# Optimization experiments

Hardware: AMD Instinct MI355X
Metric: run time of the kernel (lower is better)

Reference implementation:

```python
import jax, jax.numpy as jnp
import numpy as np

B, D, SL, N, H, LL = 2, 128, 1024, 64, 4, 4
LN_EPS = 1e-5
DIST_EPS = 1e-8


def _ln(x, g, b):
    m = x.mean(-1, keepdims=True)
    v = ((x - m) ** 2).mean(-1, keepdims=True)
    return (x - m) / jnp.sqrt(v + LN_EPS) * g + b


def _sla(x, qw, qb, kw, kb, vw, vb, ow, ob):
    # x: [B, R, C, D]; rank-1 scaled linear attention (head_qk_dim = 1)
    Bq, R, C, Dd = x.shape
    Hh = qw.shape[0]
    hd = Dd // Hh
    q = jnp.einsum('brcd,hd->brhc', x, qw) + qb[:, None]   # [B,R,H,C]
    k = jnp.einsum('brcd,hd->brhc', x, kw) + kb[:, None]
    q = jax.nn.elu(q) + 1.0
    k = jax.nn.elu(k) + 1.0
    q = q / q.mean(-1, keepdims=True)
    k = k / k.sum(-1, keepdims=True)
    v = (jnp.einsum('brcd,ed->brce', x, vw) + vb).reshape(Bq, R, C, Hh, hd)
    v = v.transpose(0, 1, 3, 2, 4)                         # [B,R,H,C,hd]
    ktv = jnp.einsum('brhc,brhce->brhe', k, v)             # [B,R,H,hd]
    V = jnp.einsum('brhc,brhe->brche', q, ktv)             # [B,R,C,H,hd]
    V = V.reshape(Bq, R, C, Dd)
    return jnp.einsum('brcd,ed->brce', V, ow) + ob


def _forward(x, rq_w, rq_b, rk_w, rk_b, rv_w, rv_b, ro_w, ro_b,
             cq_w, cq_b, ck_w, ck_b, cv_w, cv_b, co_w, co_b,
             ln_r_g, ln_r_b, ln_c_g, ln_c_b, ln_f_g, ln_f_b,
             f1_w, f1_b, f2_w, f2_b):
    y = x.transpose(0, 2, 3, 1)   # [B, L, N, D] channels-last

    def layer(y, p):
        (rqw, rqb, rkw, rkb, rvw, rvb, row_, rob,
         cqw, cqb, ckw, ckb, cvw, cvb, cow, cob,
         lrg, lrb, lcg, lcb, lfg, lfb, f1w, f1b, f2w, f2b) = p
        # row attention: rows = L, cols = N
        y = y + _sla(_ln(y, lrg, lrb), rqw, rqb, rkw, rkb, rvw, rvb, row_, rob)
        # col attention: rows = N, cols = L
        hc = _ln(y, lcg, lcb).swapaxes(1, 2)
        y = y + _sla(hc, cqw, cqb, ckw, ckb, cvw, cvb, cow, cob).swapaxes(1, 2)
        # FFN (1x1 convs == pointwise linears)
        hf = _ln(y, lfg, lfb)
        hf = jax.nn.gelu(jnp.einsum('blnd,ed->blne', hf, f1w) + f1b, approximate=False)
        y = y + (jnp.einsum('blne,de->blnd', hf, f2w) + f2b)
        return y, None

    params = (rq_w, rq_b, rk_w, rk_b, rv_w, rv_b, ro_w, ro_b,
              cq_w, cq_b, ck_w, ck_b, cv_w, cv_b, co_w, co_b,
              ln_r_g, ln_r_b, ln_c_g, ln_c_b, ln_f_g, ln_f_b,
              f1_w, f1_b, f2_w, f2_b)
    y, _ = jax.lax.scan(layer, y, params)

    # Euclidean pairwise distance head (use_cls=False): mean over sites 1..L
    xb = y[:, 1:].mean(axis=1)                 # [B, N, D]
    i0, i1 = np.tril_indices(N, -1)            # lower=True, diff=True ordering
    diffs = xb[:, i0] - xb[:, i1]              # [B, n_pairs, D]
    return jnp.sqrt(jnp.sum(diffs * diffs, axis=-1) + DIST_EPS)


def setup_inputs() -> dict:
    key = jax.random.key(0)
    ks = jax.random.split(key, 12)
    s = 0.02
    z = lambda *sh: jnp.zeros(sh, jnp.float32)
    o = lambda *sh: jnp.ones(sh, jnp.float32)
    w = lambda k, sh: jax.random.normal(k, sh, jnp.float32) * s
    p = {'x': jax.random.normal(ks[0], (B, D, SL, N), jnp.float32)}
    p['rq_w'] = w(ks[1], (LL, H, D)); p['rq_b'] = z(LL, H)
    p['rk_w'] = w(ks[2], (LL, H, D)); p['rk_b'] = z(LL, H)
    p['rv_w'] = w(ks[3], (LL, D, D)); p['rv_b'] = z(LL, D)
    p['ro_w'] = w(ks[4], (LL, D, D)); p['ro_b'] = z(LL, D)
    p['cq_w'] = w(ks[5], (LL, H, D)); p['cq_b'] = z(LL, H)
    p['ck_w'] = w(ks[6], (LL, H, D)); p['ck_b'] = z(LL, H)
    p['cv_w'] = w(ks[7], (LL, D, D)); p['cv_b'] = z(LL, D)
    p['co_w'] = w(ks[8], (LL, D, D)); p['co_b'] = z(LL, D)
    p['ln_r_g'] = o(LL, D); p['ln_r_b'] = z(LL, D)
    p['ln_c_g'] = o(LL, D); p['ln_c_b'] = z(LL, D)
    p['ln_f_g'] = o(LL, D); p['ln_f_b'] = z(LL, D)
    p['f1_w'] = w(ks[9], (LL, 4 * D, D)); p['f1_b'] = z(LL, 4 * D)
    p['f2_w'] = w(ks[10], (LL, D, 4 * D)); p['f2_b'] = z(LL, D)
    return p


def reference(x, rq_w, rq_b, rk_w, rk_b, rv_w, rv_b, ro_w, ro_b,
              cq_w, cq_b, ck_w, ck_b, cv_w, cv_b, co_w, co_b,
              ln_r_g, ln_r_b, ln_c_g, ln_c_b, ln_f_g, ln_f_b,
              f1_w, f1_b, f2_w, f2_b):
    return _forward(x, rq_w, rq_b, rk_w, rk_b, rv_w, rv_b, ro_w, ro_b,
                    cq_w, cq_b, ck_w, ck_b, cv_w, cv_b, co_w, co_b,
                    ln_r_g, ln_r_b, ln_c_g, ln_c_b, ln_f_g, ln_f_b,
                    f1_w, f1_b, f2_w, f2_b)
```

## Files before the change

### kernel.cpp

```cpp
#include <hip/hip_runtime.h>
#include <math.h>

#define LCNT 4

typedef float f32x4 __attribute__((ext_vector_type(4)));
typedef short bf16x8 __attribute__((ext_vector_type(8)));
typedef unsigned int u32;

__device__ __forceinline__ ushort bfr(float x){
  unsigned int b = __float_as_uint(x);
  return (ushort)((b + 0x7FFFu + ((b>>16)&1u)) >> 16);
}
__device__ __forceinline__ unsigned int pk2(float a, float b){
  return (unsigned int)bfr(a) | ((unsigned int)bfr(b)<<16);
}
__device__ __forceinline__ float bflo(u32 u){ return __uint_as_float(u<<16); }
__device__ __forceinline__ float bfhi(u32 u){ return __uint_as_float(u & 0xffff0000u); }
__device__ __forceinline__ float fast_gelu(float v){
  float v2 = v*v;
  float u = v*(-1.5957691f - 0.0713548162f*v2);
  float e = __expf(u);
  return v*__builtin_amdgcn_rcpf(1.f + e);
}
__device__ __forceinline__ void gl_lds16(const void* g, void* l){
  __builtin_amdgcn_global_load_lds(
      (const __attribute__((address_space(1))) u32*)g,
      (__attribute__((address_space(3))) u32*)l, 16, 0, 0);
}

__global__ __launch_bounds__(256) void k_transpose(const float* __restrict__ x,
                                                   float* __restrict__ y){
  int g = blockIdx.x;
  int b = g >> 10, l = g & 1023;
  __shared__ float sh[128*65];
  for (int idx = threadIdx.x; idx < 128*64; idx += 256){
    int d = idx >> 6, n = idx & 63;
    sh[d*65+n] = x[(((size_t)b*128 + d)*1024 + l)*64 + n];
  }
  __syncthreads();
  for (int idx = threadIdx.x; idx < 128*64; idx += 256){
    int n = idx >> 7, d = idx & 127;
    y[((size_t)g*64 + n)*128 + d] = sh[d*65+n];
  }
}

__global__ __launch_bounds__(256) void k_cvt(const float* __restrict__ src,
                                             ushort* __restrict__ dst, int n4){
  int i = blockIdx.x*256 + threadIdx.x;
  if (i < n4){
    float4 v = ((const float4*)src)[i];
    ushort4 p; p.x=bfr(v.x); p.y=bfr(v.y); p.z=bfr(v.z); p.w=bfr(v.w);
    ((ushort4*)dst)[i] = p;
  }
}

#define HSTRB 136
__global__ __launch_bounds__(256) void k_row(
    float* __restrict__ y,
    const float* __restrict__ rqw, const float* __restrict__ rqb,
    const float* __restrict__ rkw, const float* __restrict__ rkb,
    const float* __restrict__ rvw, const float* __restrict__ rvb,
    const float* __restrict__ roW, const float* __restrict__ rob,
    const float* __restrict__ lrg, const float* __restrict__ lrb,
    const float* __restrict__ cqw, const float* __restrict__ cqb,
    const float* __restrict__ ckw, const float* __restrict__ ckb,
    const float* __restrict__ lcg, const float* __restrict__ lcb,
    float2* __restrict__ stats,
    float* __restrict__ qout, float* __restrict__ kout)
{
  int g = blockIdx.x;
  __shared__ __align__(16) ushort sh_h[64*HSTRB];
  __shared__ __align__(16) float sh_w4[2048];
  __shared__ float sh_q[256], sh_k[256];
  __shared__ __align__(16) float sh_hkP[512];
  __shared__ __align__(16) float sh_ktv[128];
  int tid = threadIdx.x;
  int wid = tid>>6, ln = tid&63;

  {
    const float* wsrc = (wid==0)?rqw:(wid==1)?rkw:(wid==2)?cqw:ckw;
    gl_lds16(wsrc + ln*4,       &sh_w4[wid*512]);
    gl_lds16(wsrc + 256 + ln*4, &sh_w4[wid*512 + 256]);
  }

  int ttk = tid>>2, s4 = tid&3;
  float* yr = y + ((size_t)g*64 + ttk)*128 + s4*32;
  float4 v[8];
  #pragma unroll
  for (int i=0;i<8;i++) v[i] = *(const float4*)(yr + i*4);
  float sum = 0.f;
  #pragma unroll
  for (int i=0;i<8;i++) sum += v[i].x+v[i].y+v[i].z+v[i].w;
  sum += __shfl_xor(sum,1); sum += __shfl_xor(sum,2);
  float mean = sum*(1.0f/128.0f);
  float vs = 0.f;
  #pragma unroll
  for (int i=0;i<8;i++){
    v[i].x-=mean; v[i].y-=mean; v[i].z-=mean; v[i].w-=mean;
    vs += v[i].x*v[i].x+v[i].y*v[i].y+v[i].z*v[i].z+v[i].w*v[i].w;
  }
  vs += __shfl_xor(vs,1); vs += __shfl_xor(vs,2);
  float rstd = rsqrtf(vs*(1.0f/128.0f) + 1e-5f);
  {
    const float* gp = lrg + s4*32; const float* bp = lrb + s4*32;
    ushort* hrow = &sh_h[ttk*HSTRB + s4*32];
    #pragma unroll
    for (int i=0;i<8;i++){
      float4 g4 = *(const float4*)(gp+i*4);
      float4 b4 = *(const float4*)(bp+i*4);
      uint2 o2;
      o2.x = pk2(v[i].x*rstd*g4.x+b4.x, v[i].y*rstd*g4.y+b4.y);
      o2.y = pk2(v[i].z*rstd*g4.z+b4.z, v[i].w*rstd*g4.w+b4.w);
      *(uint2*)&hrow[i*4] = o2;
    }
  }
  __syncthreads();

  int h = tid>>6, n = tid&63;
  {
    float qr = rqb[h], kr = rkb[h];
    const int4* hp = (const int4*)&sh_h[n*HSTRB];
    const float4* qwp = (const float4*)&sh_w4[h*128];
    const float4* kwp = (const float4*)&sh_w4[512 + h*128];
    #pragma unroll 4
    for (int j=0;j<16;j++){
      int4 h8 = hp[j];
      float4 qa = qwp[2*j], qb4 = qwp[2*j+1];
      float4 ka = kwp[2*j], kb4 = kwp[2*j+1];
      float h0=bflo((u32)h8.x), h1=bfhi((u32)h8.x);
      float h2=bflo((u32)h8.y), h3=bfhi((u32)h8.y);
      float h4=bflo((u32)h8.z), h5=bfhi((u32)h8.z);
      float h6=bflo((u32)h8.w), h7=bfhi((u32)h8.w);
      qr += h0*qa.x+h1*qa.y+h2*qa.z+h3*qa.w + h4*qb4.x+h5*qb4.y+h6*qb4.z+h7*qb4.w;
      kr += h0*ka.x+h1*ka.y+h2*ka.z+h3*ka.w + h4*kb4.x+h5*kb4.y+h6*kb4.z+h7*kb4.w;
    }
    qr = qr > 0.f ? qr + 1.f : __expf(qr);
    kr = kr > 0.f ? kr + 1.f : __expf(kr);
    float qs = qr; for (int m=32;m>=1;m>>=1) qs += __shfl_xor(qs, m);
    float ks = kr; for (int m=32;m>=1;m>>=1) ks += __shfl_xor(ks, m);
    sh_q[h*64+n] = qr * (64.f/qs);
    sh_k[h*64+n] = kr * (1.f/ks);
  }
  __syncthreads();
  #pragma unroll
  for (int r=0;r<2;r++){
    int idx = tid + r*256;
    int hh = idx>>7, d = idx&127;
    float acc = 0.f;
    #pragma unroll 4
    for (int nn=0;nn<64;nn++)
      acc += sh_k[hh*64+nn]*bflo((u32)sh_h[nn*HSTRB+d]);
    sh_hkP[hh*128+d] = acc;
  }
  __syncthreads();
  if (tid < 128){
    float acc = rvb[tid];
    const float4* vr = (const float4*)(rvw + (size_t)tid*128);
    const float4* hp2 = (const float4*)(sh_hkP + (tid>>5)*128);
    #pragma unroll 8
    for (int j=0;j<32;j++){
      float4 a = vr[j], bq = hp2[j];
      acc += a.x*bq.x + a.y*bq.y + a.z*bq.z + a.w*bq.w;
    }
    sh_ktv[tid] = acc;
  }
  __syncthreads();
  #pragma unroll
  for (int r=0;r<2;r++){
    int idx = tid + r*256;
    int hh = idx>>7, e = idx&127;
    float acc = 0.f;
    const float4* orow = (const float4*)(roW + (size_t)e*128 + hh*32);
    const float4* kt = (const float4*)(sh_ktv + hh*32);
    #pragma unroll
    for (int j=0;j<8;j++){
      float4 a = orow[j], bq = kt[j];
      acc += a.x*bq.x + a.y*bq.y + a.z*bq.z + a.w*bq.w;
    }
    sh_hkP[hh*128+e] = acc;
  }
  __syncthreads();
  {
    float q0=sh_q[ttk], q1=sh_q[64+ttk], q2=sh_q[128+ttk], q3=sh_q[192+ttk];
    const float4* P4 = (const float4*)sh_hkP;
    #pragma unroll
    for (int i=0;i<8;i++){
      int d4 = s4*8 + i;
      float4 p0=P4[d4], p1=P4[32+d4], p2=P4[64+d4], p3=P4[96+d4];
      float4 o4=*(const float4*)&rob[s4*32+i*4];
      v[i].x += mean + o4.x + q0*p0.x+q1*p1.x+q2*p2.x+q3*p3.x;
      v[i].y += mean + o4.y + q0*p0.y+q1*p1.y+q2*p2.y+q3*p3.y;
      v[i].z += mean + o4.z + q0*p0.z+q1*p1.z+q2*p2.z+q3*p3.z;
      v[i].w += mean + o4.w + q0*p0.w+q1*p1.w+q2*p2.w+q3*p3.w;
      *(float4*)(yr + i*4) = v[i];
    }
  }
  float sum2 = 0.f;
  #pragma unroll
  for (int i=0;i<8;i++) sum2 += v[i].x+v[i].y+v[i].z+v[i].w;
  sum2 += __shfl_xor(sum2,1); sum2 += __shfl_xor(sum2,2);
  float cmean = sum2*(1.0f/128.0f);
  float cvs = 0.f;
  #pragma unroll
  for (int i=0;i<8;i++){
    v[i].x-=cmean; v[i].y-=cmean; v[i].z-=cmean; v[i].w-=cmean;
    cvs += v[i].x*v[i].x+v[i].y*v[i].y+v[i].z*v[i].z+v[i].w*v[i].w;
  }
  cvs += __shfl_xor(cvs,1); cvs += __shfl_xor(cvs,2);
  float crstd = rsqrtf(cvs*(1.0f/128.0f) + 1e-5f);
  if (s4 == 0) stats[(size_t)g*64 + ttk] = make_float2(cmean, crstd);
  {
    const float* gp = lcg + s4*32; const float* bp = lcb + s4*32;
    ushort* hrow = &sh_h[ttk*HSTRB + s4*32];
    #pragma unroll
    for (int i=0;i<8;i++){
      float4 g4 = *(const float4*)(gp+i*4);
      float4 b4 = *(const float4*)(bp+i*4);
      uint2 o2;
      o2.x = pk2(v[i].x*crstd*g4.x+b4.x, v[i].y*crstd*g4.y+b4.y);
      o2.y = pk2(v[i].z*crstd*g4.z+b4.z, v[i].w*crstd*g4.w+b4.w);
      *(uint2*)&hrow[i*4] = o2;
    }
  }
  __syncthreads();
  {
    float qv = cqb[h], kv = ckb[h];
    const int4* hp = (const int4*)&sh_h[n*HSTRB];
    const float4* qwp = (const float4*)&sh_w4[1024 + h*128];
    const float4* kwp = (const float4*)&sh_w4[1536 + h*128];
    #pragma unroll 4
    for (int j=0;j<16;j++){
      int4 h8 = hp[j];
      float4 qa = qwp[2*j], qb4 = qwp[2*j+1];
      float4 ka = kwp[2*j], kb4 = kwp[2*j+1];
      float h0=bflo((u32)h8.x), h1=bfhi((u32)h8.x);
      float h2=bflo((u32)h8.y), h3=bfhi((u32)h8.y);
      float h4=bflo((u32)h8.z), h5=bfhi((u32)h8.z);
      float h6=bflo((u32)h8.w), h7=bfhi((u32)h8.w);
      qv += h0*qa.x+h1*qa.y+h2*qa.z+h3*qa.w + h4*qb4.x+h5*qb4.y+h6*qb4.z+h7*qb4.w;
      kv += h0*ka.x+h1*ka.y+h2*ka.z+h3*ka.w + h4*kb4.x+h5*kb4.y+h6*kb4.z+h7*kb4.w;
    }
    qv = qv > 0.f ? qv + 1.f : __expf(qv);
    kv = kv > 0.f ? kv + 1.f : __expf(kv);
    size_t o = (size_t)g*256 + tid;
    qout[o] = qv; kout[o] = kv;
  }
}

__global__ __launch_bounds__(256) void k_qsum(const float* __restrict__ qin,
                                              float* __restrict__ qsp){
  int gg = blockIdx.x;
  int c = gg&7, b = gg>>3;
  int tid = threadIdx.x;
  const float* qp = qin + ((size_t)b*1024 + c*128)*256 + tid;
  float s = 0.f;
  #pragma unroll 4
  for (int j=0;j<128;j++){ s += *qp; qp += 256; }
  qsp[(size_t)gg*256 + tid] = s;
}

__global__ __launch_bounds__(256) void k_col_s1(
    const float* __restrict__ y, const float2* __restrict__ stats,
    const float* __restrict__ kin,
    float* __restrict__ s1p, float* __restrict__ Ab, float* __restrict__ Bb)
{
  int gg = blockIdx.x;
  int s = gg & 7, n = (gg>>3) & 63, b = gg>>9;
  int tid = threadIdx.x;
  int li = tid>>7, d = tid&127;
  const float* kp = kin + (size_t)b*262144 + n;
  float a0=0.f,a1=0.f,a2=0.f,a3=0.f;
  float A0=0.f,A1=0.f,A2=0.f,A3=0.f;
  float B0=0.f,B1=0.f,B2=0.f,B3=0.f;
  for (int j=0;j<64;j++){
    int l = s*128 + 2*j + li;
    size_t t = ((size_t)(b*1024+l)*64+n);
    float2 st = stats[t];
    float w = st.y * y[t*128 + d];
    float rm = st.y*st.x;
    const float* kl = kp + (size_t)l*256;
    float k0 = kl[0], k1 = kl[64], k2 = kl[128], k3 = kl[192];
    a0 += k0*w; a1 += k1*w; a2 += k2*w; a3 += k3*w;
    A0 += k0; A1 += k1; A2 += k2; A3 += k3;
    B0 += k0*rm; B1 += k1*rm; B2 += k2*rm; B3 += k3*rm;
  }
  __shared__ float shr[512];
  __shared__ float sAB[8];
  if (li == 1){
    shr[0*128+d]=a0; shr[1*128+d]=a1; shr[2*128+d]=a2; shr[3*128+d]=a3;
    if (d==0){ sAB[0]=A0; sAB[1]=A1; sAB[2]=A2; sAB[3]=A3;
               sAB[4]=B0; sAB[5]=B1; sAB[6]=B2; sAB[7]=B3; }
  }
  __syncthreads();
  if (li == 0){
    float* out = s1p + (size_t)gg*512;
    out[0*128+d] = a0 + shr[0*128+d];
    out[1*128+d] = a1 + shr[1*128+d];
    out[2*128+d] = a2 + shr[2*128+d];
    out[3*128+d] = a3 + shr[3*128+d];
    if (d==0){
      Ab[gg*4+0]=A0+sAB[0]; Ab[gg*4+1]=A1+sAB[1];
      Ab[gg*4+2]=A2+sAB[2]; Ab[gg*4+3]=A3+sAB[3];
      Bb[gg*4+0]=B0+sAB[4]; Bb[gg*4+1]=B1+sAB[5];
      Bb[gg*4+2]=B2+sAB[6]; Bb[gg*4+3]=B3+sAB[7];
    }
  }
}

__global__ __launch_bounds__(256) void k_col_ktvP(
    const float* __restrict__ s1p,
    const float* __restrict__ Ab, const float* __restrict__ Bb,
    const float* __restrict__ qsp,
    const float* __restrict__ vw, const float* __restrict__ vb,
    const float* __restrict__ ow,
    const float* __restrict__ lcg, const float* __restrict__ lcb,
    float* __restrict__ Pout)
{
  int gg = blockIdx.x;
  int b = gg>>6, n = gg&63;
  __shared__ float sh_hk[512];
  __shared__ float sh_ktv[128];
  __shared__ float sh_A[4], sh_B[4], sh_qs[4];
  int tid = threadIdx.x;
  #pragma unroll
  for (int r = 0; r < 2; r++){
    int idx = tid + r*256;
    float acc = 0.f;
    #pragma unroll
    for (int s = 0; s < 8; s++) acc += s1p[((size_t)gg*8 + s)*512 + idx];
    sh_hk[idx] = acc;
  }
  if (tid < 4){
    float a=0.f, bb=0.f, q=0.f;
    #pragma unroll
    for (int s = 0; s < 8; s++){ a += Ab[(gg*8+s)*4+tid]; bb += Bb[(gg*8+s)*4+tid]; }
    #pragma unroll
    for (int c = 0; c < 8; c++) q += qsp[((b*8+c)<<8) + (tid<<6) + n];
    sh_A[tid]=a; sh_B[tid]=bb; sh_qs[tid] = 1024.f/q;
  }
  __syncthreads();
  #pragma unroll
  for (int r = 0; r < 2; r++){
    int idx = tid + r*256;
    int h = idx>>7, d = idx&127;
    sh_hk[idx] = lcg[d]*((sh_hk[idx]-sh_B[h])/sh_A[h]) + lcb[d];
  }
  __syncthreads();
  if (tid < 128){
    float acc = vb[tid];
    const float* vr = vw + (size_t)tid*128;
    const float* hp2 = sh_hk + (tid>>5)*128;
    #pragma unroll 4
    for (int d = 0; d < 128; d++) acc += vr[d]*hp2[d];
    sh_ktv[tid] = acc;
  }
  __syncthreads();
  #pragma unroll
  for (int r = 0; r < 2; r++){
    int idx = tid + r*256;
    int hh = idx >> 7, e = idx & 127;
    float acc = 0.f;
    const float* orow = ow + (size_t)e*128 + hh*32;
    #pragma unroll 4
    for (int j = 0; j < 32; j++) acc += orow[j]*sh_ktv[hh*32+j];
    Pout[(size_t)gg*512 + hh*128 + e] = acc * sh_qs[hh];
  }
}

__global__ __launch_bounds__(512, 4) void k_ffn(
    float* __restrict__ y,
    const float* __restrict__ qbuf, const float* __restrict__ Pb,
    const float* __restrict__ cob,
    const float* __restrict__ gam, const float* __restrict__ bet,
    const ushort* __restrict__ w1b, const float* __restrict__ b1,
    const ushort* __restrict__ w2b, const float* __restrict__ b2)
{
  __shared__ __align__(16) ushort pool[29952];
  ushort* sW1 = pool;
  ushort* sW2 = pool + 8192;
  ushort* sH  = pool + 16384;
  ushort* sHf = pool + 25088;
  float*  sF  = (float*)pool;
  int tid = threadIdx.x;
  int g = blockIdx.x;
  size_t tb = (size_t)g*64;

  int wid = tid>>6, ln = tid&63;
  int lr = ln&15, gq = ln>>4;
  int wt = wid>>1, we = wid&1;
  int t0 = wt*16;

  #pragma unroll
  for (int i = 0; i < 2; i++){
    int row = wid*8 + i*4 + (ln>>4);
    gl_lds16(w1b + (size_t)row*128 + (((ln&15) ^ (row&7))<<3),
             &sW1[(wid*8 + i*4)*128]);
  }
  #pragma unroll
  for (int i = 0; i < 2; i++){
    int row = wid*16 + i*8 + (ln>>3);
    gl_lds16(w2b + (size_t)row*512 + (((ln&7) ^ (row&7))<<3),
             &sW2[(wid*16 + i*8)*64]);
  }

  int ttk = tid>>3, s8 = tid&7;
  float* yr = y + (tb+ttk)*128 + s8*16;
  float4 v[4];
  float fmean;
  {
    #pragma unroll
    for (int i = 0; i < 4; i++) v[i] = *(const float4*)(yr + i*4);
    const float* qp = qbuf + (size_t)g*256 + ttk;
    float q0 = qp[0], q1 = qp[64], q2 = qp[128], q3 = qp[192];
    const float* pr = Pb + ((size_t)((g>>10)*64 + ttk))*512 + s8*16;
    #pragma unroll
    for (int i = 0; i < 4; i++){
      float4 p0 = *(const float4*)(pr + i*4);
      float4 p1 = *(const float4*)(pr + 128 + i*4);
      float4 p2 = *(const float4*)(pr + 256 + i*4);
      float4 p3 = *(const float4*)(pr + 384 + i*4);
      float4 c4 = *(const float4*)&cob[s8*16 + i*4];
      v[i].x += c4.x + q0*p0.x+q1*p1.x+q2*p2.x+q3*p3.x;
      v[i].y += c4.y + q0*p0.y+q1*p1.y+q2*p2.y+q3*p3.y;
      v[i].z += c4.z + q0*p0.z+q1*p1.z+q2*p2.z+q3*p3.z;
      v[i].w += c4.w + q0*p0.w+q1*p1.w+q2*p2.w+q3*p3.w;
    }
    float sum = 0.f;
    #pragma unroll
    for (int i = 0; i < 4; i++) sum += v[i].x+v[i].y+v[i].z+v[i].w;
    sum += __shfl_xor(sum,1); sum += __shfl_xor(sum,2); sum += __shfl_xor(sum,4);
    fmean = sum*(1.0f/128.0f);
    float vs = 0.f;
    #pragma unroll
    for (int i = 0; i < 4; i++){
      v[i].x-=fmean; v[i].y-=fmean; v[i].z-=fmean; v[i].w-=fmean;
      vs += v[i].x*v[i].x+v[i].y*v[i].y+v[i].z*v[i].z+v[i].w*v[i].w;
    }
    vs += __shfl_xor(vs,1); vs += __shfl_xor(vs,2); vs += __shfl_xor(vs,4);
    float rstd = rsqrtf(vs*(1.0f/128.0f) + 1e-5f);
    const float* gp = gam + s8*16; const float* bp = bet + s8*16;
    #pragma unroll
    for (int i = 0; i < 2; i++){
      float4 ga = *(const float4*)(gp + i*8),     gb = *(const float4*)(gp + i*8 + 4);
      float4 ba = *(const float4*)(bp + i*8),     bb = *(const float4*)(bp + i*8 + 4);
      float4 va = v[i*2], vb2 = v[i*2+1];
      int4 o;
      o.x = (int)pk2(va.x*rstd*ga.x+ba.x,  va.y*rstd*ga.y+ba.y);
      o.y = (int)pk2(va.z*rstd*ga.z+ba.z,  va.w*rstd*ga.w+ba.w);
      o.z = (int)pk2(vb2.x*rstd*gb.x+bb.x, vb2.y*rstd*gb.y+bb.y);
      o.w = (int)pk2(vb2.z*rstd*gb.z+bb.z, vb2.w*rstd*gb.w+bb.w);
      *(int4*)&sH[ttk*136 + s8*16 + i*8] = o;
    }
  }
  __syncthreads();

  f32x4 acc2[4] = {};

  for (int c = 0; c < 8; c++){
    f32x4 acc1[2] = {};
    #pragma unroll
    for (int ks = 0; ks < 4; ks++){
      bf16x8 bfv = *(const bf16x8*)&sH[(t0+lr)*136 + ks*32 + gq*8];
      #pragma unroll
      for (int i = 0; i < 2; i++){
        int er = we*32 + i*16 + lr;
        bf16x8 afv = *(const bf16x8*)&sW1[er*128 + ((((ks<<2)|gq) ^ (lr&7))<<3)];
        acc1[i] = __builtin_amdgcn_mfma_f32_16x16x32_bf16(afv, bfv, acc1[i], 0, 0, 0);
      }
    }
    #pragma unroll
    for (int i = 0; i < 2; i++){
      float4 bb = *(const float4*)&b1[c*64 + we*32 + i*16 + gq*4];
      ushort4 pk;
      pk.x = bfr(fast_gelu(acc1[i][0] + bb.x));
      pk.y = bfr(fast_gelu(acc1[i][1] + bb.y));
      pk.z = bfr(fast_gelu(acc1[i][2] + bb.z));
      pk.w = bfr(fast_gelu(acc1[i][3] + bb.w));
      *(ushort4*)&sHf[(t0+lr)*72 + we*32 + i*16 + gq*4] = pk;
    }
    __syncthreads();
    if (c < 7){
      #pragma unroll
      for (int i = 0; i < 2; i++){
        int row = wid*8 + i*4 + (ln>>4);
        gl_lds16(w1b + (size_t)(c+1)*8192 + (size_t)row*128 + (((ln&15) ^ (row&7))<<3),
                 &sW1[(wid*8 + i*4)*128]);
      }
    }
    #pragma unroll
    for (int ks = 0; ks < 2; ks++){
      bf16x8 bfv = *(const bf16x8*)&sHf[(t0+lr)*72 + ks*32 + gq*8];
      #pragma unroll
      for (int j = 0; j < 4; j++){
        int dr = we*64 + j*16 + lr;
        bf16x8 afv = *(const bf16x8*)&sW2[dr*64 + ((((ks<<2)|gq) ^ (lr&7))<<3)];
        acc2[j] = __builtin_amdgcn_mfma_f32_16x16x32_bf16(afv, bfv, acc2[j], 0, 0, 0);
      }
    }
    __syncthreads();
    if (c < 7){
      #pragma unroll
      for (int i = 0; i < 2; i++){
        int row = wid*16 + i*8 + (ln>>3);
        gl_lds16(w2b + (size_t)row*512 + (c+1)*64 + (((ln&7) ^ (row&7))<<3),
                 &sW2[(wid*16 + i*8)*64]);
      }
    }
  }

  #pragma unroll
  for (int j = 0; j < 4; j++){
    float4 fo; fo.x=acc2[j][0]; fo.y=acc2[j][1]; fo.z=acc2[j][2]; fo.w=acc2[j][3];
    *(float4*)&sF[(t0+lr)*132 + we*64 + j*16 + gq*4] = fo;
  }
  __syncthreads();
  #pragma unroll
  for (int i = 0; i < 4; i++){
    float4 f = *(const float4*)&sF[ttk*132 + s8*16 + i*4];
    float4 b4 = *(const float4*)&b2[s8*16 + i*4];
    float4 o;
    o.x = v[i].x + fmean + f.x + b4.x;
    o.y = v[i].y + fmean + f.y + b4.y;
    o.z = v[i].z + fmean + f.z + b4.z;
    o.w = v[i].w + fmean + f.w + b4.w;
    *(float4*)(yr + i*4) = o;
  }
}

__global__ __launch_bounds__(128) void k_xbp(const float* __restrict__ y,
                                             float* __restrict__ xbq){
  int gg = blockIdx.x;
  int s = gg & 3, n = (gg>>2) & 63, b = gg>>8;
  int d = threadIdx.x;
  float acc = 0.f;
  int l0 = s*256 + (s==0 ? 1 : 0);
  const float* p = y + (((size_t)b*1024 + l0)*64 + n)*128 + d;
  for (int l = l0; l < s*256+256; l++){ acc += *p; p += 64*128; }
  xbq[(size_t)gg*128 + d] = acc;
}
__global__ __launch_bounds__(128) void k_xbr(const float* __restrict__ xbq,
                                             float* __restrict__ xb){
  int gg = blockIdx.x;
  int d = threadIdx.x;
  const float* q = xbq + (size_t)gg*512;
  xb[(size_t)gg*128 + d] = (q[d] + q[128+d] + q[256+d] + q[384+d]) * (1.0f/1023.0f);
}

__global__ __launch_bounds__(64) void k_dist(const float* __restrict__ xb,
                                             float* __restrict__ out){
  int p = blockIdx.x;
  int b = p >= 2016 ? 1 : 0;
  int pr = p - b*2016;
  int i0 = (int)((1.0f + sqrtf(1.0f + 8.0f*(float)pr))*0.5f);
  while (i0*(i0-1)/2 > pr) i0--;
  while ((i0+1)*i0/2 <= pr) i0++;
  int i1 = pr - i0*(i0-1)/2;
  int lane = threadIdx.x;
  const float* xa = xb + ((size_t)b*64 + i0)*128;
  const float* xc = xb + ((size_t)b*64 + i1)*128;
  float d0 = xa[lane]-xc[lane], d1 = xa[lane+64]-xc[lane+64];
  float s = d0*d0 + d1*d1;
  for (int m=32;m>=1;m>>=1) s += __shfl_xor(s, m);
  if (lane == 0) out[p] = sqrtf(s + 1e-8f);
}

extern "C" void kernel_launch(void* const* d_in, const int* in_sizes, int n_in,
                              void* d_out, int out_size, void* d_ws, size_t ws_size,
                              hipStream_t stream){
  const float* x    = (const float*)d_in[0];
  const float* rq_w = (const float*)d_in[1];  const float* rq_b = (const float*)d_in[2];
  const float* rk_w = (const float*)d_in[3];  const float* rk_b = (const float*)d_in[4];
  const float* rv_w = (const float*)d_in[5];  const float* rv_b = (const float*)d_in[6];
  const float* ro_w = (const float*)d_in[7];  const float* ro_b = (const float*)d_in[8];
  const float* cq_w = (const float*)d_in[9];  const float* cq_b = (const float*)d_in[10];
  const float* ck_w = (const float*)d_in[11]; const float* ck_b = (const float*)d_in[12];
  const float* cv_w = (const float*)d_in[13]; const float* cv_b = (const float*)d_in[14];
  const float* co_w = (const float*)d_in[15]; const float* co_b = (const float*)d_in[16];
  const float* lrg  = (const float*)d_in[17]; const float* lrb  = (const float*)d_in[18];
  const float* lcg  = (const float*)d_in[19]; const float* lcb  = (const float*)d_in[20];
  const float* lfg  = (const float*)d_in[21]; const float* lfb  = (const float*)d_in[22];
  const float* f1w  = (const float*)d_in[23]; const float* f1b  = (const float*)d_in[24];
  const float* f2w  = (const float*)d_in[25]; const float* f2b  = (const float*)d_in[26];

  float* ws = (float*)d_ws;
  float*  y   = ws;
  float2* st  = (float2*)(ws + 16777216);
  float*  qb_ = ws + 17039360;
  float*  kb_ = ws + 17563648;
  float*  Pb  = ws + 18087936;
  float*  s1p = ws + 19136512;
  float*  xb  = ws + 19661824;
  ushort* w1b = (ushort*)(ws + 19678208);
  ushort* w2b = (ushort*)(ws + 19809280);
  float*  xbq = ws + 19940352;
  float*  Ab  = ws + 20005888;
  float*  Bb  = ws + 20009984;
  float*  qsp = ws + 20014080;

  k_transpose<<<dim3(2048), dim3(256), 0, stream>>>(x, y);
  k_cvt<<<dim3(256), dim3(256), 0, stream>>>(f1w, w1b, 65536);
  k_cvt<<<dim3(256), dim3(256), 0, stream>>>(f2w, w2b, 65536);
  for (int l = 0; l < LCNT; l++){
    k_row<<<dim3(2048), dim3(256), 0, stream>>>(y,
        rq_w + l*512, rq_b + l*4, rk_w + l*512, rk_b + l*4,
        rv_w + (size_t)l*16384, rv_b + l*128, ro_w + (size_t)l*16384, ro_b + l*128,
        lrg + l*128, lrb + l*128,
        cq_w + l*512, cq_b + l*4, ck_w + l*512, ck_b + l*4,
        lcg + l*128, lcb + l*128,
        st, qb_, kb_);
    k_qsum<<<dim3(16), dim3(256), 0, stream>>>(qb_, qsp);
    k_col_s1<<<dim3(1024), dim3(256), 0, stream>>>(y, st, kb_, s1p, Ab, Bb);
    k_col_ktvP<<<dim3(128), dim3(256), 0, stream>>>(s1p, Ab, Bb, qsp,
        cv_w + (size_t)l*16384, cv_b + l*128, co_w + (size_t)l*16384,
        lcg + l*128, lcb + l*128, Pb);
    k_ffn<<<dim3(2048), dim3(512), 0, stream>>>(y, qb_, Pb, co_b + l*128,
        lfg + l*128, lfb + l*128,
        w1b + (size_t)l*65536, f1b + l*512, w2b + (size_t)l*65536, f2b + l*128);
  }
  k_xbp<<<dim3(512), dim3(128), 0, stream>>>(y, xbq);
  k_xbr<<<dim3(128), dim3(128), 0, stream>>>(xbq, xb);
  k_dist<<<dim3(4032), dim3(64), 0, stream>>>(xb, (float*)d_out);
}
```

Before: 1.049 ms.

## Widen row kernel to 512 threads and fold q-sum into column reduction

The row-attention kernel now runs 512 threads per block. Each row is split across 8 lanes instead of 4, and the two-pass loops over 512 elements become single passes, with half the threads idle during the per-head q/k projection. The separate k_qsum kernel is removed. Column q sums are accumulated inside k_col_s1 alongside the k statistics and reduced in k_col_ktvP, which saves one launch per layer and a serial 16-block reduction. The trade-off is extra global reads of q in k_col_s1 and lower per-thread work in k_row, which may or may not improve latency hiding.

```diff
diff --git a/kernel.cpp b/kernel.cpp
--- a/kernel.cpp
+++ b/kernel.cpp
@@ -55,7 +55,7 @@
 }
 
 #define HSTRB 136
-__global__ __launch_bounds__(256) void k_row(
+__global__ __launch_bounds__(512, 4) void k_row(
     float* __restrict__ y,
     const float* __restrict__ rqw, const float* __restrict__ rqb,
     const float* __restrict__ rkw, const float* __restrict__ rkb,
@@ -78,46 +78,49 @@
   int wid = tid>>6, ln = tid&63;
 
   {
-    const float* wsrc = (wid==0)?rqw:(wid==1)?rkw:(wid==2)?cqw:ckw;
-    gl_lds16(wsrc + ln*4,       &sh_w4[wid*512]);
-    gl_lds16(wsrc + 256 + ln*4, &sh_w4[wid*512 + 256]);
-  }
-
-  int ttk = tid>>2, s4 = tid&3;
-  float* yr = y + ((size_t)g*64 + ttk)*128 + s4*32;
-  float4 v[8];
-  #pragma unroll
-  for (int i=0;i<8;i++) v[i] = *(const float4*)(yr + i*4);
-  float sum = 0.f;
-  #pragma unroll
-  for (int i=0;i<8;i++) sum += v[i].x+v[i].y+v[i].z+v[i].w;
-  sum += __shfl_xor(sum,1); sum += __shfl_xor(sum,2);
-  float mean = sum*(1.0f/128.0f);
-  float vs = 0.f;
-  #pragma unroll
-  for (int i=0;i<8;i++){
-    v[i].x-=mean; v[i].y-=mean; v[i].z-=mean; v[i].w-=mean;
-    vs += v[i].x*v[i].x+v[i].y*v[i].y+v[i].z*v[i].z+v[i].w*v[i].w;
-  }
-  vs += __shfl_xor(vs,1); vs += __shfl_xor(vs,2);
-  float rstd = rsqrtf(vs*(1.0f/128.0f) + 1e-5f);
+    const float* wsrc = (wid<2)?rqw:(wid<4)?rkw:(wid<6)?cqw:ckw;
+    gl_lds16(wsrc + (wid&1)*256 + ln*4, &sh_w4[(size_t)wid*256]);
+  }
+
+  int ttk = tid>>3, s8 = tid&7;
+  float* yr = y + ((size_t)g*64 + ttk)*128 + s8*16;
+  float4 v[4];
+  float rmean;
   {
-    const float* gp = lrg + s4*32; const float* bp = lrb + s4*32;
-    ushort* hrow = &sh_h[ttk*HSTRB + s4*32];
-    #pragma unroll
-    for (int i=0;i<8;i++){
-      float4 g4 = *(const float4*)(gp+i*4);
-      float4 b4 = *(const float4*)(bp+i*4);
-      uint2 o2;
-      o2.x = pk2(v[i].x*rstd*g4.x+b4.x, v[i].y*rstd*g4.y+b4.y);
-      o2.y = pk2(v[i].z*rstd*g4.z+b4.z, v[i].w*rstd*g4.w+b4.w);
-      *(uint2*)&hrow[i*4] = o2;
-    }
-  }
-  __syncthreads();
-
-  int h = tid>>6, n = tid&63;
-  {
+    #pragma unroll
+    for (int i = 0; i < 4; i++) v[i] = *(const float4*)(yr + i*4);
+    float sum = 0.f;
+    #pragma unroll
+    for (int i = 0; i < 4; i++) sum += v[i].x+v[i].y+v[i].z+v[i].w;
+    sum += __shfl_xor(sum,1); sum += __shfl_xor(sum,2); sum += __shfl_xor(sum,4);
+    rmean = sum*(1.0f/128.0f);
+    float vs = 0.f;
+    #pragma unroll
+    for (int i = 0; i < 4; i++){
+      v[i].x-=rmean; v[i].y-=rmean; v[i].z-=rmean; v[i].w-=rmean;
+      vs += v[i].x*v[i].x+v[i].y*v[i].y+v[i].z*v[i].z+v[i].w*v[i].w;
+    }
+    vs += __shfl_xor(vs,1); vs += __shfl_xor(vs,2); vs += __shfl_xor(vs,4);
+    float rstd = rsqrtf(vs*(1.0f/128.0f) + 1e-5f);
+    const float* gp = lrg + s8*16; const float* bp = lrb + s8*16;
+    ushort* hrow = &sh_h[ttk*HSTRB + s8*16];
+    #pragma unroll
+    for (int i = 0; i < 2; i++){
+      float4 ga = *(const float4*)(gp + i*8),  gb = *(const float4*)(gp + i*8 + 4);
+      float4 ba = *(const float4*)(bp + i*8),  bb = *(const float4*)(bp + i*8 + 4);
+      float4 va = v[i*2], vb2 = v[i*2+1];
+      int4 o;
+      o.x = (int)pk2(va.x*rstd*ga.x+ba.x,  va.y*rstd*ga.y+ba.y);
+      o.y = (int)pk2(va.z*rstd*ga.z+ba.z,  va.w*rstd*ga.w+ba.w);
+      o.z = (int)pk2(vb2.x*rstd*gb.x+bb.x, vb2.y*rstd*gb.y+bb.y);
+      o.w = (int)pk2(vb2.z*rstd*gb.z+bb.z, vb2.w*rstd*gb.w+bb.w);
+      *(int4*)&hrow[i*8] = o;
+    }
+  }
+  __syncthreads();
+
+  if (tid < 256){
+    int h = tid>>6, n = tid&63;
     float qr = rqb[h], kr = rkb[h];
     const int4* hp = (const int4*)&sh_h[n*HSTRB];
     const float4* qwp = (const float4*)&sh_w4[h*128];
@@ -142,10 +145,8 @@
     sh_k[h*64+n] = kr * (1.f/ks);
   }
   __syncthreads();
-  #pragma unroll
-  for (int r=0;r<2;r++){
-    int idx = tid + r*256;
-    int hh = idx>>7, d = idx&127;
+  {
+    int hh = tid>>7, d = tid&127;
     float acc = 0.f;
     #pragma unroll 4
     for (int nn=0;nn<64;nn++)
@@ -165,10 +166,8 @@
     sh_ktv[tid] = acc;
   }
   __syncthreads();
-  #pragma unroll
-  for (int r=0;r<2;r++){
-    int idx = tid + r*256;
-    int hh = idx>>7, e = idx&127;
+  {
+    int hh = tid>>7, e = tid&127;
     float acc = 0.f;
     const float4* orow = (const float4*)(roW + (size_t)e*128 + hh*32);
     const float4* kt = (const float4*)(sh_ktv + hh*32);
@@ -182,48 +181,53 @@
   __syncthreads();
   {
     float q0=sh_q[ttk], q1=sh_q[64+ttk], q2=sh_q[128+ttk], q3=sh_q[192+ttk];
-    const float4* P4 = (const float4*)sh_hkP;
-    #pragma unroll
-    for (int i=0;i<8;i++){
-      int d4 = s4*8 + i;
-      float4 p0=P4[d4], p1=P4[32+d4], p2=P4[64+d4], p3=P4[96+d4];
-      float4 o4=*(const float4*)&rob[s4*32+i*4];
-      v[i].x += mean + o4.x + q0*p0.x+q1*p1.x+q2*p2.x+q3*p3.x;
-      v[i].y += mean + o4.y + q0*p0.y+q1*p1.y+q2*p2.y+q3*p3.y;
-      v[i].z += mean + o4.z + q0*p0.z+q1*p1.z+q2*p2.z+q3*p3.z;
-      v[i].w += mean + o4.w + q0*p0.w+q1*p1.w+q2*p2.w+q3*p3.w;
+    #pragma unroll
+    for (int i=0;i<4;i++){
+      float4 p0 = *(const float4*)&sh_hkP[s8*16 + i*4];
+      float4 p1 = *(const float4*)&sh_hkP[128 + s8*16 + i*4];
+      float4 p2 = *(const float4*)&sh_hkP[256 + s8*16 + i*4];
+      float4 p3 = *(const float4*)&sh_hkP[384 + s8*16 + i*4];
+      float4 o4 = *(const float4*)&rob[s8*16 + i*4];
+      v[i].x += rmean + o4.x + q0*p0.x+q1*p1.x+q2*p2.x+q3*p3.x;
+      v[i].y += rmean + o4.y + q0*p0.y+q1*p1.y+q2*p2.y+q3*p3.y;
+      v[i].z += rmean + o4.z + q0*p0.z+q1*p1.z+q2*p2.z+q3*p3.z;
+      v[i].w += rmean + o4.w + q0*p0.w+q1*p1.w+q2*p2.w+q3*p3.w;
       *(float4*)(yr + i*4) = v[i];
     }
   }
-  float sum2 = 0.f;
-  #pragma unroll
-  for (int i=0;i<8;i++) sum2 += v[i].x+v[i].y+v[i].z+v[i].w;
-  sum2 += __shfl_xor(sum2,1); sum2 += __shfl_xor(sum2,2);
-  float cmean = sum2*(1.0f/128.0f);
-  float cvs = 0.f;
-  #pragma unroll
-  for (int i=0;i<8;i++){
-    v[i].x-=cmean; v[i].y-=cmean; v[i].z-=cmean; v[i].w-=cmean;
-    cvs += v[i].x*v[i].x+v[i].y*v[i].y+v[i].z*v[i].z+v[i].w*v[i].w;
-  }
-  cvs += __shfl_xor(cvs,1); cvs += __shfl_xor(cvs,2);
-  float crstd = rsqrtf(cvs*(1.0f/128.0f) + 1e-5f);
-  if (s4 == 0) stats[(size_t)g*64 + ttk] = make_float2(cmean, crstd);
   {
-    const float* gp = lcg + s4*32; const float* bp = lcb + s4*32;
-    ushort* hrow = &sh_h[ttk*HSTRB + s4*32];
-    #pragma unroll
-    for (int i=0;i<8;i++){
-      float4 g4 = *(const float4*)(gp+i*4);
-      float4 b4 = *(const float4*)(bp+i*4);
-      uint2 o2;
-      o2.x = pk2(v[i].x*crstd*g4.x+b4.x, v[i].y*crstd*g4.y+b4.y);
-      o2.y = pk2(v[i].z*crstd*g4.z+b4.z, v[i].w*crstd*g4.w+b4.w);
-      *(uint2*)&hrow[i*4] = o2;
-    }
-  }
-  __syncthreads();
-  {
+    float sum2 = 0.f;
+    #pragma unroll
+    for (int i=0;i<4;i++) sum2 += v[i].x+v[i].y+v[i].z+v[i].w;
+    sum2 += __shfl_xor(sum2,1); sum2 += __shfl_xor(sum2,2); sum2 += __shfl_xor(sum2,4);
+    float cmean = sum2*(1.0f/128.0f);
+    float cvs = 0.f;
+    #pragma unroll
+    for (int i=0;i<4;i++){
+      v[i].x-=cmean; v[i].y-=cmean; v[i].z-=cmean; v[i].w-=cmean;
+      cvs += v[i].x*v[i].x+v[i].y*v[i].y+v[i].z*v[i].z+v[i].w*v[i].w;
+    }
+    cvs += __shfl_xor(cvs,1); cvs += __shfl_xor(cvs,2); cvs += __shfl_xor(cvs,4);
+    float crstd = rsqrtf(cvs*(1.0f/128.0f) + 1e-5f);
+    if (s8 == 0) stats[(size_t)g*64 + ttk] = make_float2(cmean, crstd);
+    const float* gp = lcg + s8*16; const float* bp = lcb + s8*16;
+    ushort* hrow = &sh_h[ttk*HSTRB + s8*16];
+    #pragma unroll
+    for (int i = 0; i < 2; i++){
+      float4 ga = *(const float4*)(gp + i*8),  gb = *(const float4*)(gp + i*8 + 4);
+      float4 ba = *(const float4*)(bp + i*8),  bb = *(const float4*)(bp + i*8 + 4);
+      float4 va = v[i*2], vb2 = v[i*2+1];
+      int4 o;
+      o.x = (int)pk2(va.x*crstd*ga.x+ba.x,  va.y*crstd*ga.y+ba.y);
+      o.y = (int)pk2(va.z*crstd*ga.z+ba.z,  va.w*crstd*ga.w+ba.w);
+      o.z = (int)pk2(vb2.x*crstd*gb.x+bb.x, vb2.y*crstd*gb.y+bb.y);
+      o.w = (int)pk2(vb2.z*crstd*gb.z+bb.z, vb2.w*crstd*gb.w+bb.w);
+      *(int4*)&hrow[i*8] = o;
+    }
+  }
+  __syncthreads();
+  if (tid < 256){
+    int h = tid>>6, n = tid&63;
     float qv = cqb[h], kv = ckb[h];
     const int4* hp = (const int4*)&sh_h[n*HSTRB];
     const float4* qwp = (const float4*)&sh_w4[1024 + h*128];
@@ -247,31 +251,22 @@
   }
 }
 
-__global__ __launch_bounds__(256) void k_qsum(const float* __restrict__ qin,
-                                              float* __restrict__ qsp){
-  int gg = blockIdx.x;
-  int c = gg&7, b = gg>>3;
-  int tid = threadIdx.x;
-  const float* qp = qin + ((size_t)b*1024 + c*128)*256 + tid;
-  float s = 0.f;
-  #pragma unroll 4
-  for (int j=0;j<128;j++){ s += *qp; qp += 256; }
-  qsp[(size_t)gg*256 + tid] = s;
-}
-
 __global__ __launch_bounds__(256) void k_col_s1(
     const float* __restrict__ y, const float2* __restrict__ stats,
-    const float* __restrict__ kin,
-    float* __restrict__ s1p, float* __restrict__ Ab, float* __restrict__ Bb)
+    const float* __restrict__ qin, const float* __restrict__ kin,
+    float* __restrict__ s1p, float* __restrict__ Ab, float* __restrict__ Bb,
+    float* __restrict__ Qb)
 {
   int gg = blockIdx.x;
   int s = gg & 7, n = (gg>>3) & 63, b = gg>>9;
   int tid = threadIdx.x;
   int li = tid>>7, d = tid&127;
   const float* kp = kin + (size_t)b*262144 + n;
+  const float* qp = qin + (size_t)b*262144 + n;
   float a0=0.f,a1=0.f,a2=0.f,a3=0.f;
   float A0=0.f,A1=0.f,A2=0.f,A3=0.f;
   float B0=0.f,B1=0.f,B2=0.f,B3=0.f;
+  float Q0=0.f,Q1=0.f,Q2=0.f,Q3=0.f;
   for (int j=0;j<64;j++){
     int l = s*128 + 2*j + li;
     size_t t = ((size_t)(b*1024+l)*64+n);
@@ -279,17 +274,20 @@
     float w = st.y * y[t*128 + d];
     float rm = st.y*st.x;
     const float* kl = kp + (size_t)l*256;
+    const float* ql = qp + (size_t)l*256;
     float k0 = kl[0], k1 = kl[64], k2 = kl[128], k3 = kl[192];
     a0 += k0*w; a1 += k1*w; a2 += k2*w; a3 += k3*w;
     A0 += k0; A1 += k1; A2 += k2; A3 += k3;
     B0 += k0*rm; B1 += k1*rm; B2 += k2*rm; B3 += k3*rm;
+    Q0 += ql[0]; Q1 += ql[64]; Q2 += ql[128]; Q3 += ql[192];
   }
   __shared__ float shr[512];
-  __shared__ float sAB[8];
+  __shared__ float sAB[12];
   if (li == 1){
     shr[0*128+d]=a0; shr[1*128+d]=a1; shr[2*128+d]=a2; shr[3*128+d]=a3;
     if (d==0){ sAB[0]=A0; sAB[1]=A1; sAB[2]=A2; sAB[3]=A3;
-               sAB[4]=B0; sAB[5]=B1; sAB[6]=B2; sAB[7]=B3; }
+               sAB[4]=B0; sAB[5]=B1; sAB[6]=B2; sAB[7]=B3;
+               sAB[8]=Q0; sAB[9]=Q1; sAB[10]=Q2; sAB[11]=Q3; }
   }
   __syncthreads();
   if (li == 0){
@@ -303,6 +301,8 @@
       Ab[gg*4+2]=A2+sAB[2]; Ab[gg*4+3]=A3+sAB[3];
       Bb[gg*4+0]=B0+sAB[4]; Bb[gg*4+1]=B1+sAB[5];
       Bb[gg*4+2]=B2+sAB[6]; Bb[gg*4+3]=B3+sAB[7];
+      Qb[gg*4+0]=Q0+sAB[8]; Qb[gg*4+1]=Q1+sAB[9];
+      Qb[gg*4+2]=Q2+sAB[10]; Qb[gg*4+3]=Q3+sAB[11];
     }
   }
 }
@@ -310,14 +310,13 @@
 __global__ __launch_bounds__(256) void k_col_ktvP(
     const float* __restrict__ s1p,
     const float* __restrict__ Ab, const float* __restrict__ Bb,
-    const float* __restrict__ qsp,
+    const float* __restrict__ Qb,
     const float* __restrict__ vw, const float* __restrict__ vb,
     const float* __restrict__ ow,
     const float* __restrict__ lcg, const float* __restrict__ lcb,
     float* __restrict__ Pout)
 {
   int gg = blockIdx.x;
-  int b = gg>>6, n = gg&63;
   __shared__ float sh_hk[512];
   __shared__ float sh_ktv[128];
   __shared__ float sh_A[4], sh_B[4], sh_qs[4];
@@ -333,9 +332,9 @@
   if (tid < 4){
     float a=0.f, bb=0.f, q=0.f;
     #pragma unroll
-    for (int s = 0; s < 8; s++){ a += Ab[(gg*8+s)*4+tid]; bb += Bb[(gg*8+s)*4+tid]; }
-    #pragma unroll
-    for (int c = 0; c < 8; c++) q += qsp[((b*8+c)<<8) + (tid<<6) + n];
+    for (int s = 0; s < 8; s++){
+      a += Ab[(gg*8+s)*4+tid]; bb += Bb[(gg*8+s)*4+tid]; q += Qb[(gg*8+s)*4+tid];
+    }
     sh_A[tid]=a; sh_B[tid]=bb; sh_qs[tid] = 1024.f/q;
   }
   __syncthreads();
@@ -595,22 +594,21 @@
   float*  xbq = ws + 19940352;
   float*  Ab  = ws + 20005888;
   float*  Bb  = ws + 20009984;
-  float*  qsp = ws + 20014080;
+  float*  Qb  = ws + 20014080;
 
   k_transpose<<<dim3(2048), dim3(256), 0, stream>>>(x, y);
   k_cvt<<<dim3(256), dim3(256), 0, stream>>>(f1w, w1b, 65536);
   k_cvt<<<dim3(256), dim3(256), 0, stream>>>(f2w, w2b, 65536);
   for (int l = 0; l < LCNT; l++){
-    k_row<<<dim3(2048), dim3(256), 0, stream>>>(y,
+    k_row<<<dim3(2048), dim3(512), 0, stream>>>(y,
         rq_w + l*512, rq_b + l*4, rk_w + l*512, rk_b + l*4,
         rv_w + (size_t)l*16384, rv_b + l*128, ro_w + (size_t)l*16384, ro_b + l*128,
         lrg + l*128, lrb + l*128,
         cq_w + l*512, cq_b + l*4, ck_w + l*512, ck_b + l*4,
         lcg + l*128, lcb + l*128,
         st, qb_, kb_);
-    k_qsum<<<dim3(16), dim3(256), 0, stream>>>(qb_, qsp);
-    k_col_s1<<<dim3(1024), dim3(256), 0, stream>>>(y, st, kb_, s1p, Ab, Bb);
-    k_col_ktvP<<<dim3(128), dim3(256), 0, stream>>>(s1p, Ab, Bb, qsp,
+    k_col_s1<<<dim3(1024), dim3(256), 0, stream>>>(y, st, qb_, kb_, s1p, Ab, Bb, Qb);
+    k_col_ktvP<<<dim3(128), dim3(256), 0, stream>>>(s1p, Ab, Bb, Qb,
         cv_w + (size_t)l*16384, cv_b + l*128, co_w + (size_t)l*16384,
         lcg + l*128, lcb + l*128, Pb);
     k_ffn<<<dim3(2048), dim3(512), 0, stream>>>(y, qb_, Pb, co_b + l*128,
```

New measurement: 984.9 us (median of 2 runs). 6.1% less time.
